# Kernel tuning notes

Hardware: AMD Instinct MI355X
Metric: run time of the kernel (lower is better)

The kernel has to match this reference:

```python
import jax, jax.numpy as jnp
import numpy as np

N = 65536   # instances (patches) in the bag
C = 512     # feature dim (mlp_dim)
P = 512     # number of prototypes (== C, required by the broadcast in the source)


def setup_inputs() -> dict:
    key = jax.random.key(0)
    k1, k2 = jax.random.split(key)
    x = jax.random.normal(k1, (1, N, C), dtype=jnp.float32)
    prototype = jax.random.normal(k2, (P, C), dtype=jnp.float32)
    return {"x": x, "prototype": prototype}


def reference(x, prototype):
    # x: (1, N, C) -> squeeze batch as in source
    xs = x[0]                                   # (N, C)
    # Euclidean cdist without materializing (P, N, C):
    # ||p - x||^2 = ||p||^2 + ||x||^2 - 2 p.x
    x_sq = jnp.sum(xs * xs, axis=1)             # (N,)
    p_sq = jnp.sum(prototype * prototype, axis=1)  # (P,)
    cross = jnp.einsum('pc,nc->pn', prototype, xs)  # (P, N)  -- the GEMM
    d2 = p_sq[:, None] + x_sq[None, :] - 2.0 * cross
    distances = jnp.sqrt(jnp.maximum(d2, 0.0))  # (P, N)
    # normalize by sqrt(C) (x.shape[1] after squeeze)
    distances = distances / jnp.sqrt(jnp.float32(C))
    inv_distances = 1.0 / distances             # (P, N)
    sum_inv = jnp.sum(inv_distances, axis=1, keepdims=True)  # (P, 1)
    weights = inv_distances / sum_inv           # (P, N)
    # weights.T: (N, P); elementwise with xs (N, C) -- valid since P == C
    x_out = weights.T * xs                      # (N, C)
    return (x_out, weights)
```

## Files before the change

### kernel.cpp

```cpp
#include <hip/hip_runtime.h>
#include <hip/hip_bf16.h>

typedef unsigned short ushort_t;
typedef __attribute__((ext_vector_type(8))) short bf16x8;
typedef __attribute__((ext_vector_type(4))) float f32x4;
typedef __attribute__((ext_vector_type(8))) unsigned short u16x8;

#define AS1 __attribute__((address_space(1)))
#define AS3 __attribute__((address_space(3)))

static __device__ __forceinline__ unsigned short f2bf(float f) {
    unsigned u = __float_as_uint(f);
    u += 0x7fffu + ((u >> 16) & 1u);
    return (unsigned short)(u >> 16);
}

static __device__ __forceinline__ u16x8 cvt8(const float4 f0, const float4 f1) {
    union { __hip_bfloat162 h2[4]; u16x8 v; } u;
    u.h2[0] = __float22bfloat162_rn(make_float2(f0.x, f0.y));
    u.h2[1] = __float22bfloat162_rn(make_float2(f0.z, f0.w));
    u.h2[2] = __float22bfloat162_rn(make_float2(f1.x, f1.y));
    u.h2[3] = __float22bfloat162_rn(make_float2(f1.z, f1.w));
    return u.v;
}

__global__ __launch_bounds__(256) void prep_kernel(
    const float* __restrict__ src, ushort_t* __restrict__ dst,
    float* __restrict__ sq)
{
    const int row  = blockIdx.x * 4 + (threadIdx.x >> 6);
    const int lane = threadIdx.x & 63;
    const float4* s = (const float4*)(src + (size_t)row * 512);
    float4 v0 = s[lane * 2 + 0];
    float4 v1 = s[lane * 2 + 1];
    float ss = v0.x*v0.x + v0.y*v0.y + v0.z*v0.z + v0.w*v0.w
             + v1.x*v1.x + v1.y*v1.y + v1.z*v1.z + v1.w*v1.w;
    #pragma unroll
    for (int m = 32; m >= 1; m >>= 1) ss += __shfl_xor(ss, m);
    if (lane == 0) sq[row] = ss;
    *(u16x8*)(dst + (size_t)row * 512 + lane * 8) = cvt8(v0, v1);
}

template<int MODE>
__global__ __launch_bounds__(256, 4) void gemm_f32(
    const ushort_t* __restrict__ pb, const float* __restrict__ x,
    const float* __restrict__ p_sq, float* __restrict__ x_sq,
    const float* __restrict__ rcp, float* __restrict__ wout,
    float* __restrict__ xout, float* __restrict__ partial, int Nn)
{
    __shared__ __align__(16) char smem[33280];
    ushort_t* As = (ushort_t*)smem;
    ushort_t* Bs = (ushort_t*)(smem + 16384);

    const int tid  = threadIdx.x;
    const int lane = tid & 63, wid = tid >> 6;
    const int wm = wid >> 1, wn = wid & 1;
    const int l15 = lane & 15, l4 = lane >> 4;

    const int nwg = gridDim.x * gridDim.y;
    const int w   = blockIdx.x + gridDim.x * blockIdx.y;
    int orig = w;
    if ((nwg & 7) == 0) orig = (w & 7) * (nwg >> 3) + (w >> 3);
    const int m0 = (orig & 3) * 128;
    const int n0 = (orig >> 2) * 128;
    const int by = orig >> 2;

    f32x4 acc[4][4] = {};
    float ssq[4] = {0.f, 0.f, 0.f, 0.f};

    for (int kt = 0; kt < 512; kt += 64) {
        #pragma unroll
        for (int it = 0; it < 4; ++it) {
            const int cbase = it * 256 + wid * 64;
            const int cid   = cbase + lane;
            const int r     = cid >> 3;
            const int cl    = (cid & 7) ^ (r & 7);
            const ushort_t* ga = pb + (size_t)(m0 + r) * 512 + kt + cl * 8;
            __builtin_amdgcn_global_load_lds((const AS1 unsigned int*)ga,
                (AS3 unsigned int*)(As + cbase * 8), 16, 0, 0);
        }
        #pragma unroll
        for (int it = 0; it < 4; ++it) {
            const int g  = it * 256 + tid;
            const int r  = g >> 3;
            const int cl = g & 7;
            const float4* src = (const float4*)(x + (size_t)(n0 + r) * 512 + kt + cl * 8);
            const float4 f0 = src[0];
            const float4 f1 = src[1];
            if (MODE == 0)
                ssq[it] += f0.x*f0.x + f0.y*f0.y + f0.z*f0.z + f0.w*f0.w
                         + f1.x*f1.x + f1.y*f1.y + f1.z*f1.z + f1.w*f1.w;
            *(u16x8*)&Bs[((size_t)(r * 8 + (cl ^ (r & 7)))) * 8] = cvt8(f0, f1);
        }
        __syncthreads();
        #pragma unroll
        for (int kk = 0; kk < 2; ++kk) {
            bf16x8 a[4], b[4];
            #pragma unroll
            for (int mi = 0; mi < 4; ++mi) {
                const int rr = wm * 64 + mi * 16 + l15;
                const int c  = kk * 4 + l4;
                a[mi] = *(const bf16x8*)&As[(rr * 8 + (c ^ (rr & 7))) * 8];
            }
            #pragma unroll
            for (int ni = 0; ni < 4; ++ni) {
                const int rr = wn * 64 + ni * 16 + l15;
                const int c  = kk * 4 + l4;
                b[ni] = *(const bf16x8*)&Bs[(rr * 8 + (c ^ (rr & 7))) * 8];
            }
            #pragma unroll
            for (int mi = 0; mi < 4; ++mi)
                #pragma unroll
                for (int ni = 0; ni < 4; ++ni)
                    acc[mi][ni] = __builtin_amdgcn_mfma_f32_16x16x32_bf16(
                        a[mi], b[ni], acc[mi][ni], 0, 0, 0);
        }
        __syncthreads();
    }

    if (MODE == 0) {
        float* xsq_s = (float*)(smem + 16384);
        #pragma unroll
        for (int it = 0; it < 4; ++it) {
            float s = ssq[it];
            s += __shfl_xor(s, 1); s += __shfl_xor(s, 2); s += __shfl_xor(s, 4);
            if ((tid & 7) == 0) {
                const int r = it * 32 + (tid >> 3);
                xsq_s[r] = s;
                x_sq[n0 + r] = s;
            }
        }
        __syncthreads();

        float psum[4][4] = {};
        #pragma unroll
        for (int mi = 0; mi < 4; ++mi) {
            const int pbase = m0 + wm * 64 + mi * 16 + l4 * 4;
            const f32x4 ps4 = *(const f32x4*)(p_sq + pbase);
            #pragma unroll
            for (int ni = 0; ni < 4; ++ni) {
                const int nl = wn * 64 + ni * 16 + l15;
                const float xs = xsq_s[nl];
                #pragma unroll
                for (int j = 0; j < 4; ++j) {
                    float d2 = ps4[j] + xs - 2.0f * acc[mi][ni][j];
                    d2 = fmaxf(d2, 1e-20f);
                    psum[mi][j] += 22.62741699796952f * rsqrtf(d2);
                }
            }
        }
        #pragma unroll
        for (int mi = 0; mi < 4; ++mi)
            #pragma unroll
            for (int j = 0; j < 4; ++j) {
                float s = psum[mi][j];
                s += __shfl_xor(s, 1); s += __shfl_xor(s, 2);
                s += __shfl_xor(s, 4); s += __shfl_xor(s, 8);
                psum[mi][j] = s;
            }
        float* sp = (float*)smem;
        if (l15 == 0) {
            #pragma unroll
            for (int mi = 0; mi < 4; ++mi)
                #pragma unroll
                for (int j = 0; j < 4; ++j)
                    sp[(wm * 64 + mi * 16 + l4 * 4 + j) * 2 + wn] = psum[mi][j];
        }
        __syncthreads();
        if (tid < 128)
            partial[(size_t)(m0 + tid) * gridDim.y + by] =
                sp[tid * 2] + sp[tid * 2 + 1];
    } else {
        #pragma unroll
        for (int mi = 0; mi < 4; ++mi) {
            const int pbase = m0 + wm * 64 + mi * 16 + l4 * 4;
            const f32x4 ps4 = *(const f32x4*)(p_sq + pbase);
            const f32x4 rc4 = *(const f32x4*)(rcp + pbase);
            #pragma unroll
            for (int ni = 0; ni < 4; ++ni) {
                const int n = n0 + wn * 64 + ni * 16 + l15;
                const float xs = x_sq[n];
                #pragma unroll
                for (int j = 0; j < 4; ++j) {
                    float d2 = ps4[j] + xs - 2.0f * acc[mi][ni][j];
                    d2 = fmaxf(d2, 1e-20f);
                    const float w5 = 22.62741699796952f * rsqrtf(d2) * rc4[j];
                    acc[mi][ni][j] = w5;
                    wout[(size_t)(pbase + j) * Nn + n] = w5;
                }
            }
        }
        float (*Tr)[65] = (float(*)[65])smem;
        const int tx = tid & 15, ty = tid >> 4;
        #pragma unroll
        for (int h = 0; h < 2; ++h) {
            __syncthreads();
            if (wm == h) {
                #pragma unroll
                for (int mi = 0; mi < 4; ++mi)
                    #pragma unroll
                    for (int ni = 0; ni < 4; ++ni)
                        #pragma unroll
                        for (int j = 0; j < 4; ++j)
                            Tr[wn * 64 + ni * 16 + l15][mi * 16 + l4 * 4 + j]
                                = acc[mi][ni][j];
            }
            __syncthreads();
            #pragma unroll
            for (int rr = 0; rr < 8; ++rr) {
                const int nl = ty + rr * 16;
                const size_t gx = (size_t)(n0 + nl) * 512 + m0 + h * 64 + tx * 4;
                const float4 xv = *(const float4*)(x + gx);
                f32x4 ov;
                ov[0] = xv.x * Tr[nl][tx * 4 + 0];
                ov[1] = xv.y * Tr[nl][tx * 4 + 1];
                ov[2] = xv.z * Tr[nl][tx * 4 + 2];
                ov[3] = xv.w * Tr[nl][tx * 4 + 3];
                *(f32x4*)(xout + gx) = ov;
            }
        }
    }
}

__global__ __launch_bounds__(256) void rowsum_kernel(
    const float* __restrict__ partial, float* __restrict__ rcp, int nb)
{
    const int p = blockIdx.x;
    const int tid = threadIdx.x;
    float s = 0.0f;
    for (int i = tid; i < nb; i += 256) s += partial[(size_t)p * nb + i];
    #pragma unroll
    for (int m = 32; m >= 1; m >>= 1) s += __shfl_xor(s, m);
    __shared__ float red[4];
    if ((tid & 63) == 0) red[tid >> 6] = s;
    __syncthreads();
    if (tid == 0) rcp[p] = 1.0f / (red[0] + red[1] + red[2] + red[3]);
}

template<int MODE>
__global__ __launch_bounds__(256) void gemm_old(
    const ushort_t* __restrict__ pb, const ushort_t* __restrict__ xb,
    const float* __restrict__ p_sq, const float* __restrict__ x_sq,
    const float* __restrict__ rcp,
    float* __restrict__ wout, float* __restrict__ partial, int Nn)
{
    __shared__ __align__(16) char smem[33280];
    ushort_t* As = (ushort_t*)smem;
    ushort_t* Bs = (ushort_t*)(smem + 16384);
    const int tid  = threadIdx.x;
    const int lane = tid & 63, wid = tid >> 6;
    const int wm = wid >> 1, wn = wid & 1;
    const int l15 = lane & 15, l4 = lane >> 4;
    const int m0 = blockIdx.x * 128;
    const int n0 = blockIdx.y * 128;
    f32x4 acc[4][4] = {};
    for (int kt = 0; kt < 512; kt += 64) {
        #pragma unroll
        for (int it = 0; it < 4; ++it) {
            const int cbase = it * 256 + wid * 64;
            const int cid   = cbase + lane;
            const int r     = cid >> 3;
            const int cl    = (cid & 7) ^ (r & 7);
            const ushort_t* ga = pb + (size_t)(m0 + r) * 512 + kt + cl * 8;
            __builtin_amdgcn_global_load_lds((const AS1 unsigned int*)ga,
                (AS3 unsigned int*)(As + cbase * 8), 16, 0, 0);
            const ushort_t* gb = xb + (size_t)(n0 + r) * 512 + kt + cl * 8;
            __builtin_amdgcn_global_load_lds((const AS1 unsigned int*)gb,
                (AS3 unsigned int*)(Bs + cbase * 8), 16, 0, 0);
        }
        __syncthreads();
        #pragma unroll
        for (int kk = 0; kk < 2; ++kk) {
            bf16x8 a[4], b[4];
            #pragma unroll
            for (int mi = 0; mi < 4; ++mi) {
                const int rr = wm * 64 + mi * 16 + l15;
                const int c  = kk * 4 + l4;
                a[mi] = *(const bf16x8*)&As[(rr * 8 + (c ^ (rr & 7))) * 8];
            }
            #pragma unroll
            for (int ni = 0; ni < 4; ++ni) {
                const int rr = wn * 64 + ni * 16 + l15;
                const int c  = kk * 4 + l4;
                b[ni] = *(const bf16x8*)&Bs[(rr * 8 + (c ^ (rr & 7))) * 8];
            }
            #pragma unroll
            for (int mi = 0; mi < 4; ++mi)
                #pragma unroll
                for (int ni = 0; ni < 4; ++ni)
                    acc[mi][ni] = __builtin_amdgcn_mfma_f32_16x16x32_bf16(
                        a[mi], b[ni], acc[mi][ni], 0, 0, 0);
        }
        __syncthreads();
    }
    if (MODE == 0) {
        float psum[4][4] = {};
        #pragma unroll
        for (int mi = 0; mi < 4; ++mi) {
            const int pbase = m0 + wm * 64 + mi * 16 + l4 * 4;
            const f32x4 ps4 = *(const f32x4*)(p_sq + pbase);
            #pragma unroll
            for (int ni = 0; ni < 4; ++ni) {
                const int n = n0 + wn * 64 + ni * 16 + l15;
                const float xs = x_sq[n];
                #pragma unroll
                for (int j = 0; j < 4; ++j) {
                    float d2 = ps4[j] + xs - 2.0f * acc[mi][ni][j];
                    d2 = fmaxf(d2, 1e-20f);
                    psum[mi][j] += 22.62741699796952f * rsqrtf(d2);
                }
            }
        }
        #pragma unroll
        for (int mi = 0; mi < 4; ++mi)
            #pragma unroll
            for (int j = 0; j < 4; ++j) {
                float s = psum[mi][j];
                s += __shfl_xor(s, 1); s += __shfl_xor(s, 2);
                s += __shfl_xor(s, 4); s += __shfl_xor(s, 8);
                psum[mi][j] = s;
            }
        float* sp = (float*)smem;
        if (l15 == 0) {
            #pragma unroll
            for (int mi = 0; mi < 4; ++mi)
                #pragma unroll
                for (int j = 0; j < 4; ++j)
                    sp[(wm * 64 + mi * 16 + l4 * 4 + j) * 2 + wn] = psum[mi][j];
        }
        __syncthreads();
        if (tid < 128)
            partial[(size_t)(m0 + tid) * gridDim.y + blockIdx.y] =
                sp[tid * 2] + sp[tid * 2 + 1];
    } else {
        #pragma unroll
        for (int mi = 0; mi < 4; ++mi) {
            const int pbase = m0 + wm * 64 + mi * 16 + l4 * 4;
            const f32x4 ps4 = *(const f32x4*)(p_sq + pbase);
            const f32x4 rc4 = *(const f32x4*)(rcp + pbase);
            #pragma unroll
            for (int ni = 0; ni < 4; ++ni) {
                const int n = n0 + wn * 64 + ni * 16 + l15;
                const float xs = x_sq[n];
                #pragma unroll
                for (int j = 0; j < 4; ++j) {
                    float d2 = ps4[j] + xs - 2.0f * acc[mi][ni][j];
                    d2 = fmaxf(d2, 1e-20f);
                    wout[(size_t)(pbase + j) * Nn + n] =
                        22.62741699796952f * rsqrtf(d2) * rc4[j];
                }
            }
        }
    }
}

__global__ __launch_bounds__(256) void finalize2_kernel(
    const float* __restrict__ x, const float* __restrict__ w,
    float* __restrict__ xout, int Nn)
{
    __shared__ float T[64][65];
    const int tid = threadIdx.x;
    const int tx = tid & 15, ty = tid >> 4;
    const int p0 = blockIdx.x * 64, n0 = blockIdx.y * 64;
    #pragma unroll
    for (int rr = 0; rr < 4; ++rr) {
        const int pl = ty + rr * 16;
        const f32x4 wv = *(const f32x4*)(w + (size_t)(p0 + pl) * Nn + n0 + tx * 4);
        T[tx * 4 + 0][pl] = wv[0];
        T[tx * 4 + 1][pl] = wv[1];
        T[tx * 4 + 2][pl] = wv[2];
        T[tx * 4 + 3][pl] = wv[3];
    }
    __syncthreads();
    #pragma unroll
    for (int rr = 0; rr < 4; ++rr) {
        const int nl = ty + rr * 16;
        const size_t ix = (size_t)(n0 + nl) * 512 + p0 + tx * 4;
        const f32x4 xv = *(const f32x4*)(x + ix);
        f32x4 ov;
        ov[0] = xv[0] * T[nl][tx * 4 + 0];
        ov[1] = xv[1] * T[nl][tx * 4 + 1];
        ov[2] = xv[2] * T[nl][tx * 4 + 2];
        ov[3] = xv[3] * T[nl][tx * 4 + 3];
        *(f32x4*)(xout + ix) = ov;
    }
}

extern "C" void kernel_launch(void* const* d_in, const int* in_sizes, int n_in,
                              void* d_out, int out_size, void* d_ws, size_t ws_size,
                              hipStream_t stream)
{
    const float* x     = (const float*)d_in[0];
    const float* proto = (const float*)d_in[1];
    const int C = 512, P = 512;
    const int N = in_sizes[0] / C;
    const int NB = N / 128;

    float* xout = (float*)d_out;
    float* wout = xout + (size_t)N * C;

    const size_t pbf_b = (size_t)P * C * 2;
    const size_t need  = pbf_b + (size_t)P * 4 + (size_t)N * 4
                       + (size_t)P * NB * 4 + (size_t)P * 4;

    if (ws_size >= need) {
        char* scr = (char*)d_ws;
        ushort_t* pbf  = (ushort_t*)scr;
        float*    p_sq = (float*)(scr + pbf_b);
        float*    x_sq = p_sq + P;
        float*    part = x_sq + N;
        float*    rcp  = part + (size_t)P * NB;

        prep_kernel<<<P / 4, 256, 0, stream>>>(proto, pbf, p_sq);
        gemm_f32<0><<<dim3(P / 128, NB), 256, 0, stream>>>(
            pbf, x, p_sq, x_sq, nullptr, nullptr, nullptr, part, N);
        rowsum_kernel<<<P, 256, 0, stream>>>(part, rcp, NB);
        gemm_f32<1><<<dim3(P / 128, NB), 256, 0, stream>>>(
            pbf, x, p_sq, x_sq, rcp, wout, xout, nullptr, N);
    } else {
        char* scr = (char*)d_out;
        const size_t xb_b = (size_t)N * C * 2;
        ushort_t* xb   = (ushort_t*)scr;
        ushort_t* pbf  = (ushort_t*)(scr + xb_b);
        float*    x_sq = (float*)(scr + xb_b + pbf_b);
        float*    p_sq = x_sq + N;
        float*    part = p_sq + P;
        float*    rcp  = (float*)d_ws;

        prep_kernel<<<N / 4, 256, 0, stream>>>(x, xb, x_sq);
        prep_kernel<<<P / 4, 256, 0, stream>>>(proto, pbf, p_sq);
        gemm_old<0><<<dim3(P / 128, NB), 256, 0, stream>>>(
            pbf, xb, p_sq, x_sq, nullptr, nullptr, part, N);
        rowsum_kernel<<<P, 256, 0, stream>>>(part, rcp, NB);
        gemm_old<2><<<dim3(P / 128, NB), 256, 0, stream>>>(
            pbf, xb, p_sq, x_sq, rcp, wout, nullptr, N);
        finalize2_kernel<<<dim3(P / 64, N / 64), 256, 0, stream>>>(
            x, wout, xout, N);
    }
}
```

Measured before the change: 171.8 us.

## Retile distance GEMM to 256x64 tiles and reuse weight output for partials

The fused distance GEMM kernels now use 256(prototype)x64(instance) tiles instead of 128x128. The fp32 x tile is loaded, squared and converted by fewer blocks per prototype range (2 instead of 4 M-blocks), which cuts redundant x reads and conversions. The row-sum partial buffer now lives in the weights output region rather than workspace, because the second pass overwrites it anyway. The cost is a larger LDS footprint (40 KB), more register pressure from 16 accumulators, and twice as many partial columns for the rowsum kernel to reduce.

```diff
diff --git a/kernel.cpp b/kernel.cpp
--- a/kernel.cpp
+++ b/kernel.cpp
@@ -42,15 +42,15 @@
 }
 
 template<int MODE>
-__global__ __launch_bounds__(256, 4) void gemm_f32(
+__global__ __launch_bounds__(256, 4) void gemm_s(
     const ushort_t* __restrict__ pb, const float* __restrict__ x,
     const float* __restrict__ p_sq, float* __restrict__ x_sq,
     const float* __restrict__ rcp, float* __restrict__ wout,
     float* __restrict__ xout, float* __restrict__ partial, int Nn)
 {
-    __shared__ __align__(16) char smem[33280];
+    __shared__ __align__(16) char smem[40960];
     ushort_t* As = (ushort_t*)smem;
-    ushort_t* Bs = (ushort_t*)(smem + 16384);
+    ushort_t* Bs = (ushort_t*)(smem + 32768);
 
     const int tid  = threadIdx.x;
     const int lane = tid & 63, wid = tid >> 6;
@@ -61,16 +61,16 @@
     const int w   = blockIdx.x + gridDim.x * blockIdx.y;
     int orig = w;
     if ((nwg & 7) == 0) orig = (w & 7) * (nwg >> 3) + (w >> 3);
-    const int m0 = (orig & 3) * 128;
-    const int n0 = (orig >> 2) * 128;
-    const int by = orig >> 2;
-
-    f32x4 acc[4][4] = {};
-    float ssq[4] = {0.f, 0.f, 0.f, 0.f};
+    const int m0 = (orig & 1) * 256;
+    const int n0 = (orig >> 1) * 64;
+    const int by = orig >> 1;
+
+    f32x4 acc[8][2] = {};
+    float ssq[2] = {0.f, 0.f};
 
     for (int kt = 0; kt < 512; kt += 64) {
         #pragma unroll
-        for (int it = 0; it < 4; ++it) {
+        for (int it = 0; it < 8; ++it) {
             const int cbase = it * 256 + wid * 64;
             const int cid   = cbase + lane;
             const int r     = cid >> 3;
@@ -80,7 +80,7 @@
                 (AS3 unsigned int*)(As + cbase * 8), 16, 0, 0);
         }
         #pragma unroll
-        for (int it = 0; it < 4; ++it) {
+        for (int it = 0; it < 2; ++it) {
             const int g  = it * 256 + tid;
             const int r  = g >> 3;
             const int cl = g & 7;
@@ -95,33 +95,29 @@
         __syncthreads();
         #pragma unroll
         for (int kk = 0; kk < 2; ++kk) {
-            bf16x8 a[4], b[4];
-            #pragma unroll
-            for (int mi = 0; mi < 4; ++mi) {
-                const int rr = wm * 64 + mi * 16 + l15;
-                const int c  = kk * 4 + l4;
-                a[mi] = *(const bf16x8*)&As[(rr * 8 + (c ^ (rr & 7))) * 8];
-            }
-            #pragma unroll
-            for (int ni = 0; ni < 4; ++ni) {
-                const int rr = wn * 64 + ni * 16 + l15;
+            bf16x8 b[2];
+            #pragma unroll
+            for (int ni = 0; ni < 2; ++ni) {
+                const int rr = wn * 32 + ni * 16 + l15;
                 const int c  = kk * 4 + l4;
                 b[ni] = *(const bf16x8*)&Bs[(rr * 8 + (c ^ (rr & 7))) * 8];
             }
             #pragma unroll
-            for (int mi = 0; mi < 4; ++mi)
-                #pragma unroll
-                for (int ni = 0; ni < 4; ++ni)
-                    acc[mi][ni] = __builtin_amdgcn_mfma_f32_16x16x32_bf16(
-                        a[mi], b[ni], acc[mi][ni], 0, 0, 0);
+            for (int mi = 0; mi < 8; ++mi) {
+                const int rr = wm * 128 + mi * 16 + l15;
+                const int c  = kk * 4 + l4;
+                const bf16x8 a = *(const bf16x8*)&As[(rr * 8 + (c ^ (rr & 7))) * 8];
+                acc[mi][0] = __builtin_amdgcn_mfma_f32_16x16x32_bf16(a, b[0], acc[mi][0], 0, 0, 0);
+                acc[mi][1] = __builtin_amdgcn_mfma_f32_16x16x32_bf16(a, b[1], acc[mi][1], 0, 0, 0);
+            }
         }
         __syncthreads();
     }
 
     if (MODE == 0) {
-        float* xsq_s = (float*)(smem + 16384);
-        #pragma unroll
-        for (int it = 0; it < 4; ++it) {
+        float* xsq_s = (float*)(smem + 32768);
+        #pragma unroll
+        for (int it = 0; it < 2; ++it) {
             float s = ssq[it];
             s += __shfl_xor(s, 1); s += __shfl_xor(s, 2); s += __shfl_xor(s, 4);
             if ((tid & 7) == 0) {
@@ -132,14 +128,14 @@
         }
         __syncthreads();
 
-        float psum[4][4] = {};
-        #pragma unroll
-        for (int mi = 0; mi < 4; ++mi) {
-            const int pbase = m0 + wm * 64 + mi * 16 + l4 * 4;
+        float psum[8][4] = {};
+        #pragma unroll
+        for (int mi = 0; mi < 8; ++mi) {
+            const int pbase = m0 + wm * 128 + mi * 16 + l4 * 4;
             const f32x4 ps4 = *(const f32x4*)(p_sq + pbase);
             #pragma unroll
-            for (int ni = 0; ni < 4; ++ni) {
-                const int nl = wn * 64 + ni * 16 + l15;
+            for (int ni = 0; ni < 2; ++ni) {
+                const int nl = wn * 32 + ni * 16 + l15;
                 const float xs = xsq_s[nl];
                 #pragma unroll
                 for (int j = 0; j < 4; ++j) {
@@ -150,7 +146,7 @@
             }
         }
         #pragma unroll
-        for (int mi = 0; mi < 4; ++mi)
+        for (int mi = 0; mi < 8; ++mi)
             #pragma unroll
             for (int j = 0; j < 4; ++j) {
                 float s = psum[mi][j];
@@ -161,24 +157,22 @@
         float* sp = (float*)smem;
         if (l15 == 0) {
             #pragma unroll
-            for (int mi = 0; mi < 4; ++mi)
+            for (int mi = 0; mi < 8; ++mi)
                 #pragma unroll
                 for (int j = 0; j < 4; ++j)
-                    sp[(wm * 64 + mi * 16 + l4 * 4 + j) * 2 + wn] = psum[mi][j];
-        }
-        __syncthreads();
-        if (tid < 128)
-            partial[(size_t)(m0 + tid) * gridDim.y + by] =
-                sp[tid * 2] + sp[tid * 2 + 1];
+                    sp[(wm * 128 + mi * 16 + l4 * 4 + j) * 2 + wn] = psum[mi][j];
+        }
+        __syncthreads();
+        partial[(size_t)(m0 + tid) * gridDim.y + by] = sp[tid * 2] + sp[tid * 2 + 1];
     } else {
         #pragma unroll
-        for (int mi = 0; mi < 4; ++mi) {
-            const int pbase = m0 + wm * 64 + mi * 16 + l4 * 4;
+        for (int mi = 0; mi < 8; ++mi) {
+            const int pbase = m0 + wm * 128 + mi * 16 + l4 * 4;
             const f32x4 ps4 = *(const f32x4*)(p_sq + pbase);
             const f32x4 rc4 = *(const f32x4*)(rcp + pbase);
             #pragma unroll
-            for (int ni = 0; ni < 4; ++ni) {
-                const int n = n0 + wn * 64 + ni * 16 + l15;
+            for (int ni = 0; ni < 2; ++ni) {
+                const int n = n0 + wn * 32 + ni * 16 + l15;
                 const float xs = x_sq[n];
                 #pragma unroll
                 for (int j = 0; j < 4; ++j) {
@@ -193,21 +187,22 @@
         float (*Tr)[65] = (float(*)[65])smem;
         const int tx = tid & 15, ty = tid >> 4;
         #pragma unroll
-        for (int h = 0; h < 2; ++h) {
+        for (int h = 0; h < 4; ++h) {
             __syncthreads();
-            if (wm == h) {
-                #pragma unroll
-                for (int mi = 0; mi < 4; ++mi)
+            if (wm == (h >> 1)) {
+                const int mb = (h & 1) * 4;
+                #pragma unroll
+                for (int mq = 0; mq < 4; ++mq)
                     #pragma unroll
-                    for (int ni = 0; ni < 4; ++ni)
+                    for (int ni = 0; ni < 2; ++ni)
                         #pragma unroll
                         for (int j = 0; j < 4; ++j)
-                            Tr[wn * 64 + ni * 16 + l15][mi * 16 + l4 * 4 + j]
-                                = acc[mi][ni][j];
+                            Tr[wn * 32 + ni * 16 + l15][mq * 16 + l4 * 4 + j]
+                                = acc[mb + mq][ni][j];
             }
             __syncthreads();
             #pragma unroll
-            for (int rr = 0; rr < 8; ++rr) {
+            for (int rr = 0; rr < 4; ++rr) {
                 const int nl = ty + rr * 16;
                 const size_t gx = (size_t)(n0 + nl) * 512 + m0 + h * 64 + tx * 4;
                 const float4 xv = *(const float4*)(x + gx);
@@ -394,28 +389,27 @@
     const float* proto = (const float*)d_in[1];
     const int C = 512, P = 512;
     const int N = in_sizes[0] / C;
-    const int NB = N / 128;
+    const int NB = N / 64;
 
     float* xout = (float*)d_out;
     float* wout = xout + (size_t)N * C;
 
     const size_t pbf_b = (size_t)P * C * 2;
-    const size_t need  = pbf_b + (size_t)P * 4 + (size_t)N * 4
-                       + (size_t)P * NB * 4 + (size_t)P * 4;
+    const size_t need  = pbf_b + (size_t)P * 4 + (size_t)N * 4 + (size_t)P * 4;
 
     if (ws_size >= need) {
         char* scr = (char*)d_ws;
         ushort_t* pbf  = (ushort_t*)scr;
         float*    p_sq = (float*)(scr + pbf_b);
         float*    x_sq = p_sq + P;
-        float*    part = x_sq + N;
-        float*    rcp  = part + (size_t)P * NB;
+        float*    rcp  = x_sq + N;
+        float*    part = wout;
 
         prep_kernel<<<P / 4, 256, 0, stream>>>(proto, pbf, p_sq);
-        gemm_f32<0><<<dim3(P / 128, NB), 256, 0, stream>>>(
+        gemm_s<0><<<dim3(2, NB), 256, 0, stream>>>(
             pbf, x, p_sq, x_sq, nullptr, nullptr, nullptr, part, N);
         rowsum_kernel<<<P, 256, 0, stream>>>(part, rcp, NB);
-        gemm_f32<1><<<dim3(P / 128, NB), 256, 0, stream>>>(
+        gemm_s<1><<<dim3(2, NB), 256, 0, stream>>>(
             pbf, x, p_sq, x_sq, rcp, wout, xout, nullptr, N);
     } else {
         char* scr = (char*)d_out;
@@ -429,10 +423,10 @@
 
         prep_kernel<<<N / 4, 256, 0, stream>>>(x, xb, x_sq);
         prep_kernel<<<P / 4, 256, 0, stream>>>(proto, pbf, p_sq);
-        gemm_old<0><<<dim3(P / 128, NB), 256, 0, stream>>>(
+        gemm_old<0><<<dim3(P / 128, N / 128), 256, 0, stream>>>(
             pbf, xb, p_sq, x_sq, nullptr, nullptr, part, N);
-        rowsum_kernel<<<P, 256, 0, stream>>>(part, rcp, NB);
-        gemm_old<2><<<dim3(P / 128, NB), 256, 0, stream>>>(
+        rowsum_kernel<<<P, 256, 0, stream>>>(part, rcp, N / 128);
+        gemm_old<2><<<dim3(P / 128, N / 128), 256, 0, stream>>>(
             pbf, xb, p_sq, x_sq, rcp, wout, nullptr, N);
         finalize2_kernel<<<dim3(P / 64, N / 64), 256, 0, stream>>>(
             x, wout, xout, N);
```

After: 187.1 us. 8.9% more time.
